# Kernel optimization log

Measured on AMD Instinct MI355X. Metric: run time of the kernel, lower is better.

The kernel has to match this reference:

```python
import jax, jax.numpy as jnp
import numpy as np

D_MODEL = 1024
N_HEADS = 16
D_K = D_MODEL // N_HEADS


def setup_inputs() -> dict:
    key = jax.random.key(0)
    kx, kq, kk, kv, ko = jax.random.split(key, 5)
    scale = 1.0 / np.sqrt(D_MODEL)
    return {
        "x": jax.random.normal(kx, (2, 2048, D_MODEL), dtype=jnp.float32),
        "W_Q": jax.random.normal(kq, (D_MODEL, D_MODEL), dtype=jnp.float32) * scale,
        "W_K": jax.random.normal(kk, (D_MODEL, D_MODEL), dtype=jnp.float32) * scale,
        "W_V": jax.random.normal(kv, (D_MODEL, D_MODEL), dtype=jnp.float32) * scale,
        "W_O": jax.random.normal(ko, (D_MODEL, D_MODEL), dtype=jnp.float32) * scale,
    }


def reference(x, W_Q, W_K, W_V, W_O) -> jnp.ndarray:
    B, S, _ = x.shape
    # Projections; weights stored as (d_model, d_model), applied as x @ W (Linear weight transposed convention folded into init)
    def heads(w):
        return jnp.einsum('bsd,de->bse', x, w).reshape(B, S, N_HEADS, D_K).transpose(0, 2, 1, 3)
    Q, K, V = heads(W_Q), heads(W_K), heads(W_V)  # (B,H,S,d_k)
    scores = jnp.einsum('bhqd,bhkd->bhqk', Q, K) / jnp.sqrt(jnp.asarray(D_K, x.dtype))
    causal_mask = jnp.triu(jnp.ones((S, S), dtype=bool), k=1)  # True above diagonal
    scores = jnp.where(causal_mask[None, None], jnp.asarray(-jnp.inf, x.dtype), scores)
    attn = jax.nn.softmax(scores, axis=-1)
    out = jnp.einsum('bhqk,bhkd->bhqd', attn, V)  # (B,H,S,d_k)
    out = out.transpose(0, 2, 1, 3).reshape(B, S, N_HEADS * D_K)
    return jnp.einsum('bsd,de->bse', out, W_O)
```

## Files before the change

### kernel.cpp

```cpp
#include <hip/hip_runtime.h>

typedef unsigned short u16;
typedef unsigned int u32;
typedef __attribute__((ext_vector_type(8))) __bf16 bf16x8;
typedef __attribute__((ext_vector_type(2))) __bf16 bf16x2;
typedef __attribute__((ext_vector_type(4))) float f32x4;
typedef __attribute__((ext_vector_type(16))) float f32x16;
typedef __attribute__((ext_vector_type(4))) u32 u32x4;

__device__ inline u16 f2bf(float f) {
  unsigned u = __builtin_bit_cast(unsigned, f);
  u += 0x7FFFu + ((u >> 16) & 1u);
  return (u16)(u >> 16);
}

__device__ inline u32 packbf(float a, float b) {
  bf16x2 t;
  t[0] = (__bf16)a;
  t[1] = (__bf16)b;
  return __builtin_bit_cast(u32, t);
}

__device__ inline void async16(const void* g, void* l) {
  __builtin_amdgcn_global_load_lds((const __attribute__((address_space(1))) void*)g,
                                   (__attribute__((address_space(3))) void*)l, 16, 0, 0);
}

__global__ __launch_bounds__(256) void xconv(const float* __restrict__ x, u16* __restrict__ xb) {
  int i = blockIdx.x * 256 + threadIdx.x;
  float4 v = ((const float4*)x)[i];
  ushort4 r;
  r.x = f2bf(v.x); r.y = f2bf(v.y); r.z = f2bf(v.z); r.w = f2bf(v.w);
  ((ushort4*)xb)[i] = r;
}

__global__ __launch_bounds__(256) void wtrans4(const float* __restrict__ W0,
                                               const float* __restrict__ W1,
                                               const float* __restrict__ W2,
                                               const float* __restrict__ W3,
                                               u16* __restrict__ WtQKV,
                                               u16* __restrict__ WtO) {
  __shared__ u16 tile[32][33];
  const int z = blockIdx.z;
  const float* W = (z == 0) ? W0 : (z == 1) ? W1 : (z == 2) ? W2 : W3;
  u16* Wt = (z < 3) ? (WtQKV + (size_t)z * 1024 * 1024) : WtO;
  const float s = (z == 0) ? 0.18033688011112042f : 1.0f;
  const int e0 = blockIdx.x * 32;
  const int d0 = blockIdx.y * 32;
  const int tx = threadIdx.x & 31;
  const int ty = threadIdx.x >> 5;
#pragma unroll
  for (int i = ty; i < 32; i += 8)
    tile[i][tx] = f2bf(W[(size_t)(d0 + i) * 1024 + e0 + tx] * s);
  __syncthreads();
#pragma unroll
  for (int i = ty; i < 32; i += 8)
    Wt[(size_t)(e0 + i) * 1024 + d0 + tx] = tile[tx][i];
}

__global__ __launch_bounds__(256) void vtrans(const u16* __restrict__ QKV, u16* __restrict__ Vtg) {
  __shared__ u16 t[32][66];
  const int tid = threadIdx.x;
  const int s0 = blockIdx.x * 32, dg0 = blockIdx.y * 64, b = blockIdx.z;
  {
    const int i = tid >> 3, c = (tid & 7) * 8;
    uint4 v = *(const uint4*)(QKV + (size_t)(b * 2048 + s0 + i) * 3072 + 2048 + dg0 + c);
    u16 tmp[8];
    *(uint4*)tmp = v;
#pragma unroll
    for (int e = 0; e < 8; ++e) t[i][c + e] = tmp[e];
  }
  __syncthreads();
  {
    const int r = tid >> 2, cg = (tid & 3) * 8;
    u16 tmp[8];
#pragma unroll
    for (int e = 0; e < 8; ++e) tmp[e] = t[cg + e][r];
    *(uint4*)(Vtg + (size_t)(b * 1024 + dg0 + r) * 2048 + s0 + cg) = *(uint4*)tmp;
  }
}

template <int OUT_BF16>
__global__ __launch_bounds__(256) void gemm_bt(const u16* __restrict__ A,
                                               const u16* __restrict__ Bt,
                                               void* __restrict__ Cp,
                                               int M, int N, int K) {
  __shared__ __align__(16) u16 As[128 * 32];
  __shared__ __align__(16) u16 Bs[128 * 32];
  const int tid = threadIdx.x;
  const int lane = tid & 63;
  const int wave = tid >> 6;
  const int lr = lane & 15;
  const int lk = (lane >> 4) * 8;
  const int wm = (wave >> 1) * 64;
  const int wn = (wave & 1) * 64;
  const int bm = blockIdx.x * 128;
  const int bn = blockIdx.y * 128;
  const int srow = lane >> 2;
  const int scol = (lane & 3) * 8;

  f32x4 acc[4][4] = {};

  for (int k0 = 0; k0 < K; k0 += 32) {
#pragma unroll
    for (int r = 0; r < 2; ++r) {
      const int chunk = r * 4 + wave;
      const int row = chunk * 16 + srow;
      async16(A + (size_t)(bm + row) * K + k0 + scol, &As[chunk * 512 + lane * 8]);
      async16(Bt + (size_t)(bn + row) * K + k0 + scol, &Bs[chunk * 512 + lane * 8]);
    }
    __syncthreads();
    bf16x8 a[4], b[4];
#pragma unroll
    for (int i = 0; i < 4; ++i) {
      a[i] = *(const bf16x8*)&As[(wm + i * 16 + lr) * 32 + lk];
      b[i] = *(const bf16x8*)&Bs[(wn + i * 16 + lr) * 32 + lk];
    }
#pragma unroll
    for (int mi = 0; mi < 4; ++mi)
#pragma unroll
      for (int ni = 0; ni < 4; ++ni)
        acc[mi][ni] = __builtin_amdgcn_mfma_f32_16x16x32_bf16(a[mi], b[ni], acc[mi][ni], 0, 0, 0);
    __syncthreads();
  }

#pragma unroll
  for (int mi = 0; mi < 4; ++mi) {
#pragma unroll
    for (int ni = 0; ni < 4; ++ni) {
      const int col = bn + wn + ni * 16 + lr;
#pragma unroll
      for (int j = 0; j < 4; ++j) {
        const int row = bm + wm + mi * 16 + (lane >> 4) * 4 + j;
        if (OUT_BF16)
          ((u16*)Cp)[(size_t)row * N + col] = f2bf(acc[mi][ni][j]);
        else
          ((float*)Cp)[(size_t)row * N + col] = acc[mi][ni][j];
      }
    }
  }
}

__global__ __launch_bounds__(512) void attn_kernel(const u16* __restrict__ QKV,
                                                   const u16* __restrict__ Vtg,
                                                   u16* __restrict__ Opart,
                                                   float* __restrict__ Lpart) {
  constexpr int S = 2048, LD = 3072;
  constexpr float MFIX = 12.0f;
  __shared__ __align__(16) u16 Ks[2][64 * 64];
  __shared__ __align__(16) u16 Vs[2][64 * 64];

  const int g = 7 - (blockIdx.x >> 1);
  const int c = blockIdx.x & 1;
  const int bh = blockIdx.y;
  const int b = bh >> 4, h = bh & 15;
  const int tid = threadIdx.x, lane = tid & 63, w = tid >> 6;
  const int l31 = lane & 31, lh = lane >> 5;

  const int qbase = g * 256 + w * 32;
  const int ktlast = 4 * g + (w >> 1);
  const int ktbeg = c * (2 * g + 2);
  const int ktend = (c + 1) * (2 * g + 2);

  const u16* qrow = QKV + (size_t)(b * S + qbase + l31) * LD + h * 64;
  bf16x8 qf[4];
#pragma unroll
  for (int cc = 0; cc < 4; ++cc) qf[cc] = *(const bf16x8*)(qrow + cc * 16 + lh * 8);

  const int r0 = tid >> 3, x0 = ((tid & 7) ^ (r0 & 7)) << 3;
  const u16* Kbase = QKV + (size_t)b * S * LD + 1024 + h * 64;
  const u16* Vbase = Vtg + (size_t)bh * 64 * 2048;

#define STAGE(buf, kt_)                                                          \
  do {                                                                           \
    async16(Kbase + (size_t)((kt_)*64 + r0) * LD + x0, &Ks[buf][tid * 8]);       \
    async16(Vbase + (size_t)r0 * 2048 + (kt_)*64 + x0, &Vs[buf][tid * 8]);       \
  } while (0)

  f32x16 o0 = {}, o1 = {};
  float l_run = 0.f;

  STAGE(0, ktbeg);

  int cur = 0;
  for (int kt = ktbeg; kt < ktend; ++kt) {
    if (kt + 1 < ktend) {
      STAGE(cur ^ 1, kt + 1);
      asm volatile("s_waitcnt vmcnt(2)" ::: "memory");
    } else {
      asm volatile("s_waitcnt vmcnt(0)" ::: "memory");
    }
    __builtin_amdgcn_s_barrier();
    __builtin_amdgcn_sched_barrier(0);

    const bool active = (kt <= ktlast);
    const bool hiA = active && ((kt < ktlast) || (w & 1));

    if (active) {
      const u16* ks = Ks[cur];
      const u16* vs = Vs[cur];

      f32x16 t0 = {}, t1 = {};
      __builtin_amdgcn_s_setprio(1);
#pragma unroll
      for (int cc = 0; cc < 4; ++cc) {
        const int ci = 2 * cc + lh;
        const bf16x8 kf0 = *(const bf16x8*)&ks[l31 * 64 + ((ci ^ (l31 & 7)) << 3)];
        t0 = __builtin_amdgcn_mfma_f32_32x32x16_bf16(kf0, qf[cc], t0, 0, 0, 0);
        if (hiA) {
          const bf16x8 kf1 = *(const bf16x8*)&ks[(32 + l31) * 64 + ((ci ^ (l31 & 7)) << 3)];
          t1 = __builtin_amdgcn_mfma_f32_32x32x16_bf16(kf1, qf[cc], t1, 0, 0, 0);
        }
      }
      __builtin_amdgcn_s_setprio(0);

      if (kt == ktlast) {
        const int kb = kt * 64 + 4 * lh;
        const int qa = qbase + l31;
#pragma unroll
        for (int r = 0; r < 16; ++r) {
          const int ko = (r & 3) + 8 * (r >> 2);
          if (kb + ko > qa) t0[r] = -3e38f;
          if (hiA && (kb + 32 + ko > qa)) t1[r] = -3e38f;
        }
      }

      f32x16 p0 = t0, p1 = t1;
#pragma unroll
      for (int r = 0; r < 16; ++r) p0[r] = exp2f(t0[r] - MFIX);
      if (hiA) {
#pragma unroll
        for (int r = 0; r < 16; ++r) p1[r] = exp2f(t1[r] - MFIX);
      }
      float v[16];
#pragma unroll
      for (int r = 0; r < 16; ++r) v[r] = hiA ? (p0[r] + p1[r]) : p0[r];
#pragma unroll
      for (int s = 8; s >= 1; s >>= 1)
#pragma unroll
        for (int r = 0; r < s; ++r) v[r] += v[r + s];
      l_run += v[0];

      u32 pk0[8], pk1[8], sw0[8], sw1[8];
#pragma unroll
      for (int j = 0; j < 8; ++j) pk0[j] = packbf(p0[2 * j], p0[2 * j + 1]);
#pragma unroll
      for (int j = 0; j < 8; ++j) sw0[j] = __shfl_xor(pk0[j], 32);
      if (hiA) {
#pragma unroll
        for (int j = 0; j < 8; ++j) pk1[j] = packbf(p1[2 * j], p1[2 * j + 1]);
#pragma unroll
        for (int j = 0; j < 8; ++j) sw1[j] = __shfl_xor(pk1[j], 32);
      }

      __builtin_amdgcn_s_setprio(1);
#define PVSTEP(kc, pk, sw)                                                             \
      {                                                                                \
        const int q4 = ((kc) & 1) * 4;                                                 \
        u32x4 wv;                                                                      \
        wv[0] = lh ? sw[q4 + 2] : pk[q4 + 0];                                          \
        wv[1] = lh ? sw[q4 + 3] : pk[q4 + 1];                                          \
        wv[2] = lh ? pk[q4 + 2] : sw[q4 + 0];                                          \
        wv[3] = lh ? pk[q4 + 3] : sw[q4 + 1];                                          \
        const bf16x8 pa = __builtin_bit_cast(bf16x8, wv);                              \
        const int ci = 2 * (kc) + lh;                                                  \
        const bf16x8 vf0 = *(const bf16x8*)&vs[l31 * 64 + ((ci ^ (l31 & 7)) << 3)];    \
        const bf16x8 vf1 = *(const bf16x8*)&vs[(32 + l31) * 64 + ((ci ^ (l31 & 7)) << 3)]; \
        o0 = __builtin_amdgcn_mfma_f32_32x32x16_bf16(pa, vf0, o0, 0, 0, 0);            \
        o1 = __builtin_amdgcn_mfma_f32_32x32x16_bf16(pa, vf1, o1, 0, 0, 0);            \
      }
      PVSTEP(0, pk0, sw0)
      PVSTEP(1, pk0, sw0)
      if (hiA) {
        PVSTEP(2, pk1, sw1)
        PVSTEP(3, pk1, sw1)
      }
#undef PVSTEP
      __builtin_amdgcn_s_setprio(0);
    }

    asm volatile("s_waitcnt lgkmcnt(0)" ::: "memory");
    __builtin_amdgcn_s_barrier();
    cur ^= 1;
  }
#undef STAGE

  u16* Oc = Opart + (size_t)c * 4096 * 1024;
#pragma unroll
  for (int r = 0; r < 16; ++r) {
    const int qo = (r & 3) + 8 * (r >> 2) + 4 * lh;
    u16* op = Oc + (size_t)(b * S + qbase + qo) * 1024 + h * 64 + l31;
    op[0] = f2bf(o0[r]);
    op[32] = f2bf(o1[r]);
  }
  const float l_tot = l_run + __shfl_xor(l_run, 32);
  if (lh == 0)
    Lpart[(size_t)c * 4096 * 16 + (size_t)(b * S + qbase + l31) * 16 + h] = l_tot;
}

__global__ __launch_bounds__(256) void combine(const u16* __restrict__ Opart,
                                               const float* __restrict__ Lpart,
                                               u16* __restrict__ Obuf) {
  const int i = blockIdx.x * 256 + threadIdx.x;
  const int row = i >> 7;
  const int cw = (i & 127) * 8;
  const int h = cw >> 6;
  const float l = Lpart[(size_t)row * 16 + h] + Lpart[(size_t)4096 * 16 + (size_t)row * 16 + h];
  const float inv = 1.0f / l;
  const bf16x8 a = *(const bf16x8*)(Opart + (size_t)row * 1024 + cw);
  const bf16x8 bq = *(const bf16x8*)(Opart + (size_t)4096 * 1024 + (size_t)row * 1024 + cw);
  u16 out[8];
#pragma unroll
  for (int j = 0; j < 8; ++j) out[j] = f2bf(((float)a[j] + (float)bq[j]) * inv);
  *(uint4*)(Obuf + (size_t)row * 1024 + cw) = *(uint4*)out;
}

extern "C" void kernel_launch(void* const* d_in, const int* in_sizes, int n_in,
                              void* d_out, int out_size, void* d_ws, size_t ws_size,
                              hipStream_t stream) {
  const float* x  = (const float*)d_in[0];
  const float* WQ = (const float*)d_in[1];
  const float* WK = (const float*)d_in[2];
  const float* WV = (const float*)d_in[3];
  const float* WO = (const float*)d_in[4];
  float* out = (float*)d_out;

  u16* xb    = (u16*)d_ws;
  u16* WtQKV = xb + (size_t)4096 * 1024;
  u16* WtO   = WtQKV + (size_t)3072 * 1024;
  u16* QKV   = WtO + (size_t)1024 * 1024;
  u16* Obuf  = QKV + (size_t)4096 * 3072;
  u16* Vtg   = Obuf + (size_t)4096 * 1024;
  u16* Opart = Vtg + (size_t)2048 * 2048;
  float* Lpart = (float*)(Opart + (size_t)2 * 4096 * 1024);

  xconv<<<4096, 256, 0, stream>>>(x, xb);
  wtrans4<<<dim3(32, 32, 4), 256, 0, stream>>>(WQ, WK, WV, WO, WtQKV, WtO);

  gemm_bt<1><<<dim3(32, 24), 256, 0, stream>>>(xb, WtQKV, QKV, 4096, 3072, 1024);
  vtrans<<<dim3(64, 16, 2), 256, 0, stream>>>(QKV, Vtg);
  attn_kernel<<<dim3(16, 32), 512, 0, stream>>>(QKV, Vtg, Opart, Lpart);
  combine<<<2048, 256, 0, stream>>>(Opart, Lpart, Obuf);
  gemm_bt<0><<<dim3(32, 8), 256, 0, stream>>>(Obuf, WtO, out, 4096, 1024, 1024);
}
```

Before: 164.9 us.

## Software-pipeline QK and softmax-PV across tiles and compute row sums via MFMA

The attention loop is restructured so the QK^T MFMAs for tile kt run alongside the softmax and PV of tile kt-1. V fragments are held in registers across iterations, and a drain step runs after the loop. Row sums are now produced by an extra MFMA against a ones vector instead of a scalar reduction. The per-warp causal skip logic is removed, so all tiles are computed and masked, which adds work on fully masked tiles. A launch-bounds occupancy hint of two blocks is also added, which raises register pressure.

```diff
diff --git a/kernel.cpp b/kernel.cpp
--- a/kernel.cpp
+++ b/kernel.cpp
@@ -141,10 +141,10 @@
   }
 }
 
-__global__ __launch_bounds__(512) void attn_kernel(const u16* __restrict__ QKV,
-                                                   const u16* __restrict__ Vtg,
-                                                   u16* __restrict__ Opart,
-                                                   float* __restrict__ Lpart) {
+__global__ __launch_bounds__(512, 2) void attn_kernel(const u16* __restrict__ QKV,
+                                                      const u16* __restrict__ Vtg,
+                                                      u16* __restrict__ Opart,
+                                                      float* __restrict__ Lpart) {
   constexpr int S = 2048, LD = 3072;
   constexpr float MFIX = 12.0f;
   __shared__ __align__(16) u16 Ks[2][64 * 64];
@@ -158,7 +158,7 @@
   const int l31 = lane & 31, lh = lane >> 5;
 
   const int qbase = g * 256 + w * 32;
-  const int ktlast = 4 * g + (w >> 1);
+  const int qa = qbase + l31;
   const int ktbeg = c * (2 * g + 2);
   const int ktend = (c + 1) * (2 * g + 2);
 
@@ -166,6 +166,13 @@
   bf16x8 qf[4];
 #pragma unroll
   for (int cc = 0; cc < 4; ++cc) qf[cc] = *(const bf16x8*)(qrow + cc * 16 + lh * 8);
+
+  bf16x8 onesf;
+  {
+    u32x4 ov;
+    ov[0] = ov[1] = ov[2] = ov[3] = 0x3F803F80u;
+    onesf = __builtin_bit_cast(bf16x8, ov);
+  }
 
   const int r0 = tid >> 3, x0 = ((tid & 7) ^ (r0 & 7)) << 3;
   const u16* Kbase = QKV + (size_t)b * S * LD + 1024 + h * 64;
@@ -178,9 +185,53 @@
   } while (0)
 
   f32x16 o0 = {}, o1 = {};
-  float l_run = 0.f;
+  f32x16 l_acc = {};
+  f32x16 tp0, tp1;
+#pragma unroll
+  for (int r = 0; r < 16; ++r) { tp0[r] = -3e38f; tp1[r] = -3e38f; }
+  bf16x8 vfp0[4], vfp1[4];
 
   STAGE(0, ktbeg);
+  asm volatile("s_waitcnt vmcnt(0)" ::: "memory");
+  __builtin_amdgcn_s_barrier();
+  __builtin_amdgcn_sched_barrier(0);
+#pragma unroll
+  for (int kc = 0; kc < 4; ++kc) {
+    const int ci = 2 * kc + lh;
+    vfp0[kc] = *(const bf16x8*)&Vs[0][l31 * 64 + ((ci ^ (l31 & 7)) << 3)];
+    vfp1[kc] = *(const bf16x8*)&Vs[0][(32 + l31) * 64 + ((ci ^ (l31 & 7)) << 3)];
+  }
+
+#define SOFTMAX_PV()                                                                   \
+  do {                                                                                 \
+    _Pragma("unroll") for (int r = 0; r < 16; ++r) {                                   \
+      tp0[r] = exp2f(tp0[r] - MFIX);                                                   \
+      tp1[r] = exp2f(tp1[r] - MFIX);                                                   \
+    }                                                                                  \
+    u32 pk0[8], pk1[8], sw0[8], sw1[8];                                                \
+    _Pragma("unroll") for (int j = 0; j < 8; ++j) {                                    \
+      pk0[j] = packbf(tp0[2 * j], tp0[2 * j + 1]);                                     \
+      pk1[j] = packbf(tp1[2 * j], tp1[2 * j + 1]);                                     \
+    }                                                                                  \
+    _Pragma("unroll") for (int j = 0; j < 8; ++j) {                                    \
+      sw0[j] = __shfl_xor(pk0[j], 32);                                                 \
+      sw1[j] = __shfl_xor(pk1[j], 32);                                                 \
+    }                                                                                  \
+    _Pragma("unroll") for (int kc = 0; kc < 4; ++kc) {                                 \
+      const u32* pk = (kc >> 1) ? pk1 : pk0;                                           \
+      const u32* sw = (kc >> 1) ? sw1 : sw0;                                           \
+      const int q4 = (kc & 1) * 4;                                                     \
+      u32x4 wv;                                                                        \
+      wv[0] = lh ? sw[q4 + 2] : pk[q4 + 0];                                            \
+      wv[1] = lh ? sw[q4 + 3] : pk[q4 + 1];                                            \
+      wv[2] = lh ? pk[q4 + 2] : sw[q4 + 0];                                            \
+      wv[3] = lh ? pk[q4 + 3] : sw[q4 + 1];                                            \
+      const bf16x8 pa = __builtin_bit_cast(bf16x8, wv);                                \
+      o0 = __builtin_amdgcn_mfma_f32_32x32x16_bf16(pa, vfp0[kc], o0, 0, 0, 0);         \
+      o1 = __builtin_amdgcn_mfma_f32_32x32x16_bf16(pa, vfp1[kc], o1, 0, 0, 0);         \
+      l_acc = __builtin_amdgcn_mfma_f32_32x32x16_bf16(pa, onesf, l_acc, 0, 0, 0);      \
+    }                                                                                  \
+  } while (0)
 
   int cur = 0;
   for (int kt = ktbeg; kt < ktend; ++kt) {
@@ -193,96 +244,46 @@
     __builtin_amdgcn_s_barrier();
     __builtin_amdgcn_sched_barrier(0);
 
-    const bool active = (kt <= ktlast);
-    const bool hiA = active && ((kt < ktlast) || (w & 1));
-
-    if (active) {
-      const u16* ks = Ks[cur];
-      const u16* vs = Vs[cur];
-
-      f32x16 t0 = {}, t1 = {};
-      __builtin_amdgcn_s_setprio(1);
-#pragma unroll
-      for (int cc = 0; cc < 4; ++cc) {
-        const int ci = 2 * cc + lh;
-        const bf16x8 kf0 = *(const bf16x8*)&ks[l31 * 64 + ((ci ^ (l31 & 7)) << 3)];
-        t0 = __builtin_amdgcn_mfma_f32_32x32x16_bf16(kf0, qf[cc], t0, 0, 0, 0);
-        if (hiA) {
-          const bf16x8 kf1 = *(const bf16x8*)&ks[(32 + l31) * 64 + ((ci ^ (l31 & 7)) << 3)];
-          t1 = __builtin_amdgcn_mfma_f32_32x32x16_bf16(kf1, qf[cc], t1, 0, 0, 0);
-        }
+    const u16* ks = Ks[cur];
+    const u16* vs = Vs[cur];
+
+    f32x16 tc0 = {}, tc1 = {};
+#pragma unroll
+    for (int cc = 0; cc < 4; ++cc) {
+      const int ci = 2 * cc + lh;
+      const bf16x8 kf0 = *(const bf16x8*)&ks[l31 * 64 + ((ci ^ (l31 & 7)) << 3)];
+      const bf16x8 kf1 = *(const bf16x8*)&ks[(32 + l31) * 64 + ((ci ^ (l31 & 7)) << 3)];
+      tc0 = __builtin_amdgcn_mfma_f32_32x32x16_bf16(kf0, qf[cc], tc0, 0, 0, 0);
+      tc1 = __builtin_amdgcn_mfma_f32_32x32x16_bf16(kf1, qf[cc], tc1, 0, 0, 0);
+    }
+    {
+      const int kb = kt * 64 + 4 * lh;
+#pragma unroll
+      for (int r = 0; r < 16; ++r) {
+        const int ko = kb + (r & 3) + 8 * (r >> 2);
+        tc0[r] = (ko > qa) ? -3e38f : tc0[r];
+        tc1[r] = (ko + 32 > qa) ? -3e38f : tc1[r];
       }
-      __builtin_amdgcn_s_setprio(0);
-
-      if (kt == ktlast) {
-        const int kb = kt * 64 + 4 * lh;
-        const int qa = qbase + l31;
-#pragma unroll
-        for (int r = 0; r < 16; ++r) {
-          const int ko = (r & 3) + 8 * (r >> 2);
-          if (kb + ko > qa) t0[r] = -3e38f;
-          if (hiA && (kb + 32 + ko > qa)) t1[r] = -3e38f;
-        }
-      }
-
-      f32x16 p0 = t0, p1 = t1;
-#pragma unroll
-      for (int r = 0; r < 16; ++r) p0[r] = exp2f(t0[r] - MFIX);
-      if (hiA) {
-#pragma unroll
-        for (int r = 0; r < 16; ++r) p1[r] = exp2f(t1[r] - MFIX);
-      }
-      float v[16];
-#pragma unroll
-      for (int r = 0; r < 16; ++r) v[r] = hiA ? (p0[r] + p1[r]) : p0[r];
-#pragma unroll
-      for (int s = 8; s >= 1; s >>= 1)
-#pragma unroll
-        for (int r = 0; r < s; ++r) v[r] += v[r + s];
-      l_run += v[0];
-
-      u32 pk0[8], pk1[8], sw0[8], sw1[8];
-#pragma unroll
-      for (int j = 0; j < 8; ++j) pk0[j] = packbf(p0[2 * j], p0[2 * j + 1]);
-#pragma unroll
-      for (int j = 0; j < 8; ++j) sw0[j] = __shfl_xor(pk0[j], 32);
-      if (hiA) {
-#pragma unroll
-        for (int j = 0; j < 8; ++j) pk1[j] = packbf(p1[2 * j], p1[2 * j + 1]);
-#pragma unroll
-        for (int j = 0; j < 8; ++j) sw1[j] = __shfl_xor(pk1[j], 32);
-      }
-
-      __builtin_amdgcn_s_setprio(1);
-#define PVSTEP(kc, pk, sw)                                                             \
-      {                                                                                \
-        const int q4 = ((kc) & 1) * 4;                                                 \
-        u32x4 wv;                                                                      \
-        wv[0] = lh ? sw[q4 + 2] : pk[q4 + 0];                                          \
-        wv[1] = lh ? sw[q4 + 3] : pk[q4 + 1];                                          \
-        wv[2] = lh ? pk[q4 + 2] : sw[q4 + 0];                                          \
-        wv[3] = lh ? pk[q4 + 3] : sw[q4 + 1];                                          \
-        const bf16x8 pa = __builtin_bit_cast(bf16x8, wv);                              \
-        const int ci = 2 * (kc) + lh;                                                  \
-        const bf16x8 vf0 = *(const bf16x8*)&vs[l31 * 64 + ((ci ^ (l31 & 7)) << 3)];    \
-        const bf16x8 vf1 = *(const bf16x8*)&vs[(32 + l31) * 64 + ((ci ^ (l31 & 7)) << 3)]; \
-        o0 = __builtin_amdgcn_mfma_f32_32x32x16_bf16(pa, vf0, o0, 0, 0, 0);            \
-        o1 = __builtin_amdgcn_mfma_f32_32x32x16_bf16(pa, vf1, o1, 0, 0, 0);            \
-      }
-      PVSTEP(0, pk0, sw0)
-      PVSTEP(1, pk0, sw0)
-      if (hiA) {
-        PVSTEP(2, pk1, sw1)
-        PVSTEP(3, pk1, sw1)
-      }
-#undef PVSTEP
-      __builtin_amdgcn_s_setprio(0);
-    }
+    }
+
+    SOFTMAX_PV();
+
+#pragma unroll
+    for (int kc = 0; kc < 4; ++kc) {
+      const int ci = 2 * kc + lh;
+      vfp0[kc] = *(const bf16x8*)&vs[l31 * 64 + ((ci ^ (l31 & 7)) << 3)];
+      vfp1[kc] = *(const bf16x8*)&vs[(32 + l31) * 64 + ((ci ^ (l31 & 7)) << 3)];
+    }
+    tp0 = tc0;
+    tp1 = tc1;
 
     asm volatile("s_waitcnt lgkmcnt(0)" ::: "memory");
     __builtin_amdgcn_s_barrier();
     cur ^= 1;
   }
+
+  SOFTMAX_PV();
+#undef SOFTMAX_PV
 #undef STAGE
 
   u16* Oc = Opart + (size_t)c * 4096 * 1024;
@@ -293,9 +294,13 @@
     op[0] = f2bf(o0[r]);
     op[32] = f2bf(o1[r]);
   }
-  const float l_tot = l_run + __shfl_xor(l_run, 32);
-  if (lh == 0)
-    Lpart[(size_t)c * 4096 * 16 + (size_t)(b * S + qbase + l31) * 16 + h] = l_tot;
+  if (l31 == 0) {
+#pragma unroll
+    for (int r = 0; r < 16; ++r) {
+      const int qo = (r & 3) + 8 * (r >> 2) + 4 * lh;
+      Lpart[(size_t)c * 4096 * 16 + (size_t)(b * S + qbase + qo) * 16 + h] = l_acc[r];
+    }
+  }
 }
 
 __global__ __launch_bounds__(256) void combine(const u16* __restrict__ Opart,
```

New measurement: 170.0 us. 1.03x slower.

## Give each attention wave 64 query rows to reuse K/V fragments

Applied to the files above, without the earlier changes.

Halves the attention block to 256 threads (4 waves), with each wave now owning 64 query rows as two 32-row halves instead of 32 rows. Each K and V fragment read from LDS then feeds twice as many MFMAs. Each thread issues twice as many async copies per stage, and the causal mask on the diagonal tile is simplified to a local comparison. In exchange, per-wave register pressure roughly doubles (four output accumulators, two Q fragment sets) and each block has fewer waves, which may reduce occupancy and latency hiding.

```diff
diff --git a/kernel.cpp b/kernel.cpp
--- a/kernel.cpp
+++ b/kernel.cpp
@@ -141,10 +141,10 @@
   }
 }
 
-__global__ __launch_bounds__(512) void attn_kernel(const u16* __restrict__ QKV,
-                                                   const u16* __restrict__ Vtg,
-                                                   u16* __restrict__ Opart,
-                                                   float* __restrict__ Lpart) {
+__global__ __launch_bounds__(256, 2) void attn_kernel(const u16* __restrict__ QKV,
+                                                      const u16* __restrict__ Vtg,
+                                                      u16* __restrict__ Opart,
+                                                      float* __restrict__ Lpart) {
   constexpr int S = 2048, LD = 3072;
   constexpr float MFIX = 12.0f;
   __shared__ __align__(16) u16 Ks[2][64 * 64];
@@ -157,28 +157,55 @@
   const int tid = threadIdx.x, lane = tid & 63, w = tid >> 6;
   const int l31 = lane & 31, lh = lane >> 5;
 
-  const int qbase = g * 256 + w * 32;
-  const int ktlast = 4 * g + (w >> 1);
+  const int qbase = g * 256 + w * 64;
+  const int ktlast = 4 * g + w;
   const int ktbeg = c * (2 * g + 2);
   const int ktend = (c + 1) * (2 * g + 2);
 
-  const u16* qrow = QKV + (size_t)(b * S + qbase + l31) * LD + h * 64;
-  bf16x8 qf[4];
-#pragma unroll
-  for (int cc = 0; cc < 4; ++cc) qf[cc] = *(const bf16x8*)(qrow + cc * 16 + lh * 8);
-
-  const int r0 = tid >> 3, x0 = ((tid & 7) ^ (r0 & 7)) << 3;
+  bf16x8 qf[2][4];
+#pragma unroll
+  for (int qh = 0; qh < 2; ++qh) {
+    const u16* qrow = QKV + (size_t)(b * S + qbase + qh * 32 + l31) * LD + h * 64;
+#pragma unroll
+    for (int cc = 0; cc < 4; ++cc) qf[qh][cc] = *(const bf16x8*)(qrow + cc * 16 + lh * 8);
+  }
+
+  const int c0 = tid, c1 = tid + 256;
+  const int r0 = c0 >> 3, x0 = ((c0 & 7) ^ (r0 & 7)) << 3;
+  const int r1 = c1 >> 3, x1 = ((c1 & 7) ^ (r1 & 7)) << 3;
   const u16* Kbase = QKV + (size_t)b * S * LD + 1024 + h * 64;
   const u16* Vbase = Vtg + (size_t)bh * 64 * 2048;
 
 #define STAGE(buf, kt_)                                                          \
   do {                                                                           \
-    async16(Kbase + (size_t)((kt_)*64 + r0) * LD + x0, &Ks[buf][tid * 8]);       \
-    async16(Vbase + (size_t)r0 * 2048 + (kt_)*64 + x0, &Vs[buf][tid * 8]);       \
+    async16(Kbase + (size_t)((kt_)*64 + r0) * LD + x0, &Ks[buf][c0 * 8]);        \
+    async16(Kbase + (size_t)((kt_)*64 + r1) * LD + x1, &Ks[buf][c1 * 8]);        \
+    async16(Vbase + (size_t)r0 * 2048 + (kt_)*64 + x0, &Vs[buf][c0 * 8]);        \
+    async16(Vbase + (size_t)r1 * 2048 + (kt_)*64 + x1, &Vs[buf][c1 * 8]);        \
   } while (0)
 
-  f32x16 o0 = {}, o1 = {};
-  float l_run = 0.f;
+  f32x16 o00 = {}, o01 = {}, o10 = {}, o11 = {};
+  float l0 = 0.f, l1 = 0.f;
+
+#define TREE16(dst, arr)                                                         \
+  do {                                                                           \
+    float v_[16];                                                                \
+    _Pragma("unroll") for (int r_ = 0; r_ < 16; ++r_) v_[r_] = (arr)[r_];        \
+    _Pragma("unroll") for (int s_ = 8; s_ >= 1; s_ >>= 1)                        \
+      _Pragma("unroll") for (int r_ = 0; r_ < s_; ++r_) v_[r_] += v_[r_ + s_];   \
+    dst += v_[0];                                                                \
+  } while (0)
+
+#define MAKE_PA(pa, pk, sw, q4)                                                  \
+  bf16x8 pa;                                                                     \
+  {                                                                              \
+    u32x4 wv_;                                                                   \
+    wv_[0] = lh ? (sw)[(q4) + 2] : (pk)[(q4) + 0];                               \
+    wv_[1] = lh ? (sw)[(q4) + 3] : (pk)[(q4) + 1];                               \
+    wv_[2] = lh ? (pk)[(q4) + 2] : (sw)[(q4) + 0];                               \
+    wv_[3] = lh ? (pk)[(q4) + 3] : (sw)[(q4) + 1];                               \
+    pa = __builtin_bit_cast(bf16x8, wv_);                                        \
+  }
 
   STAGE(0, ktbeg);
 
@@ -186,7 +213,7 @@
   for (int kt = ktbeg; kt < ktend; ++kt) {
     if (kt + 1 < ktend) {
       STAGE(cur ^ 1, kt + 1);
-      asm volatile("s_waitcnt vmcnt(2)" ::: "memory");
+      asm volatile("s_waitcnt vmcnt(4)" ::: "memory");
     } else {
       asm volatile("s_waitcnt vmcnt(0)" ::: "memory");
     }
@@ -194,88 +221,100 @@
     __builtin_amdgcn_sched_barrier(0);
 
     const bool active = (kt <= ktlast);
-    const bool hiA = active && ((kt < ktlast) || (w & 1));
-
     if (active) {
+      const bool full = (kt < ktlast);
       const u16* ks = Ks[cur];
       const u16* vs = Vs[cur];
 
-      f32x16 t0 = {}, t1 = {};
+      f32x16 t00 = {}, t10 = {}, t01 = {}, t11 = {};
       __builtin_amdgcn_s_setprio(1);
 #pragma unroll
       for (int cc = 0; cc < 4; ++cc) {
         const int ci = 2 * cc + lh;
         const bf16x8 kf0 = *(const bf16x8*)&ks[l31 * 64 + ((ci ^ (l31 & 7)) << 3)];
-        t0 = __builtin_amdgcn_mfma_f32_32x32x16_bf16(kf0, qf[cc], t0, 0, 0, 0);
-        if (hiA) {
-          const bf16x8 kf1 = *(const bf16x8*)&ks[(32 + l31) * 64 + ((ci ^ (l31 & 7)) << 3)];
-          t1 = __builtin_amdgcn_mfma_f32_32x32x16_bf16(kf1, qf[cc], t1, 0, 0, 0);
+        const bf16x8 kf1 = *(const bf16x8*)&ks[(32 + l31) * 64 + ((ci ^ (l31 & 7)) << 3)];
+        t00 = __builtin_amdgcn_mfma_f32_32x32x16_bf16(kf0, qf[0][cc], t00, 0, 0, 0);
+        t01 = __builtin_amdgcn_mfma_f32_32x32x16_bf16(kf0, qf[1][cc], t01, 0, 0, 0);
+        if (full) t10 = __builtin_amdgcn_mfma_f32_32x32x16_bf16(kf1, qf[0][cc], t10, 0, 0, 0);
+        t11 = __builtin_amdgcn_mfma_f32_32x32x16_bf16(kf1, qf[1][cc], t11, 0, 0, 0);
+      }
+      __builtin_amdgcn_s_setprio(0);
+
+      if (!full) {
+#pragma unroll
+        for (int r = 0; r < 16; ++r) {
+          const int ko = (r & 3) + 8 * (r >> 2) + 4 * lh;
+          if (ko > l31) { t00[r] = -3e38f; t11[r] = -3e38f; }
         }
       }
+
+      u32 pk0[8], pk1[8], sw0[8], sw1[8];
+
+#pragma unroll
+      for (int r = 0; r < 16; ++r) t00[r] = exp2f(t00[r] - MFIX);
+#pragma unroll
+      for (int r = 0; r < 16; ++r) t01[r] = exp2f(t01[r] - MFIX);
+      TREE16(l0, t00);
+      TREE16(l1, t01);
+#pragma unroll
+      for (int j = 0; j < 8; ++j) {
+        pk0[j] = packbf(t00[2 * j], t00[2 * j + 1]);
+        pk1[j] = packbf(t01[2 * j], t01[2 * j + 1]);
+      }
+#pragma unroll
+      for (int j = 0; j < 8; ++j) {
+        sw0[j] = __shfl_xor(pk0[j], 32);
+        sw1[j] = __shfl_xor(pk1[j], 32);
+      }
+      __builtin_amdgcn_s_setprio(1);
+#pragma unroll
+      for (int kc = 0; kc < 2; ++kc) {
+        const int q4 = kc * 4;
+        MAKE_PA(pa0, pk0, sw0, q4)
+        MAKE_PA(pa1, pk1, sw1, q4)
+        const int ci = 2 * kc + lh;
+        const bf16x8 vd0 = *(const bf16x8*)&vs[l31 * 64 + ((ci ^ (l31 & 7)) << 3)];
+        const bf16x8 vd1 = *(const bf16x8*)&vs[(32 + l31) * 64 + ((ci ^ (l31 & 7)) << 3)];
+        o00 = __builtin_amdgcn_mfma_f32_32x32x16_bf16(pa0, vd0, o00, 0, 0, 0);
+        o01 = __builtin_amdgcn_mfma_f32_32x32x16_bf16(pa0, vd1, o01, 0, 0, 0);
+        o10 = __builtin_amdgcn_mfma_f32_32x32x16_bf16(pa1, vd0, o10, 0, 0, 0);
+        o11 = __builtin_amdgcn_mfma_f32_32x32x16_bf16(pa1, vd1, o11, 0, 0, 0);
+      }
       __builtin_amdgcn_s_setprio(0);
 
-      if (kt == ktlast) {
-        const int kb = kt * 64 + 4 * lh;
-        const int qa = qbase + l31;
-#pragma unroll
-        for (int r = 0; r < 16; ++r) {
-          const int ko = (r & 3) + 8 * (r >> 2);
-          if (kb + ko > qa) t0[r] = -3e38f;
-          if (hiA && (kb + 32 + ko > qa)) t1[r] = -3e38f;
+      if (full) {
+#pragma unroll
+        for (int r = 0; r < 16; ++r) t10[r] = exp2f(t10[r] - MFIX);
+        TREE16(l0, t10);
+#pragma unroll
+        for (int j = 0; j < 8; ++j) pk0[j] = packbf(t10[2 * j], t10[2 * j + 1]);
+#pragma unroll
+        for (int j = 0; j < 8; ++j) sw0[j] = __shfl_xor(pk0[j], 32);
+      }
+#pragma unroll
+      for (int r = 0; r < 16; ++r) t11[r] = exp2f(t11[r] - MFIX);
+      TREE16(l1, t11);
+#pragma unroll
+      for (int j = 0; j < 8; ++j) pk1[j] = packbf(t11[2 * j], t11[2 * j + 1]);
+#pragma unroll
+      for (int j = 0; j < 8; ++j) sw1[j] = __shfl_xor(pk1[j], 32);
+
+      __builtin_amdgcn_s_setprio(1);
+#pragma unroll
+      for (int kc = 0; kc < 2; ++kc) {
+        const int q4 = kc * 4;
+        MAKE_PA(pa1, pk1, sw1, q4)
+        const int ci = 2 * (kc + 2) + lh;
+        const bf16x8 vd0 = *(const bf16x8*)&vs[l31 * 64 + ((ci ^ (l31 & 7)) << 3)];
+        const bf16x8 vd1 = *(const bf16x8*)&vs[(32 + l31) * 64 + ((ci ^ (l31 & 7)) << 3)];
+        if (full) {
+          MAKE_PA(pa0, pk0, sw0, q4)
+          o00 = __builtin_amdgcn_mfma_f32_32x32x16_bf16(pa0, vd0, o00, 0, 0, 0);
+          o01 = __builtin_amdgcn_mfma_f32_32x32x16_bf16(pa0, vd1, o01, 0, 0, 0);
         }
-      }
-
-      f32x16 p0 = t0, p1 = t1;
-#pragma unroll
-      for (int r = 0; r < 16; ++r) p0[r] = exp2f(t0[r] - MFIX);
-      if (hiA) {
-#pragma unroll
-        for (int r = 0; r < 16; ++r) p1[r] = exp2f(t1[r] - MFIX);
-      }
-      float v[16];
-#pragma unroll
-      for (int r = 0; r < 16; ++r) v[r] = hiA ? (p0[r] + p1[r]) : p0[r];
-#pragma unroll
-      for (int s = 8; s >= 1; s >>= 1)
-#pragma unroll
-        for (int r = 0; r < s; ++r) v[r] += v[r + s];
-      l_run += v[0];
-
-      u32 pk0[8], pk1[8], sw0[8], sw1[8];
-#pragma unroll
-      for (int j = 0; j < 8; ++j) pk0[j] = packbf(p0[2 * j], p0[2 * j + 1]);
-#pragma unroll
-      for (int j = 0; j < 8; ++j) sw0[j] = __shfl_xor(pk0[j], 32);
-      if (hiA) {
-#pragma unroll
-        for (int j = 0; j < 8; ++j) pk1[j] = packbf(p1[2 * j], p1[2 * j + 1]);
-#pragma unroll
-        for (int j = 0; j < 8; ++j) sw1[j] = __shfl_xor(pk1[j], 32);
-      }
-
-      __builtin_amdgcn_s_setprio(1);
-#define PVSTEP(kc, pk, sw)                                                             \
-      {                                                                                \
-        const int q4 = ((kc) & 1) * 4;                                                 \
-        u32x4 wv;                                                                      \
-        wv[0] = lh ? sw[q4 + 2] : pk[q4 + 0];                                          \
-        wv[1] = lh ? sw[q4 + 3] : pk[q4 + 1];                                          \
-        wv[2] = lh ? pk[q4 + 2] : sw[q4 + 0];                                          \
-        wv[3] = lh ? pk[q4 + 3] : sw[q4 + 1];                                          \
-        const bf16x8 pa = __builtin_bit_cast(bf16x8, wv);                              \
-        const int ci = 2 * (kc) + lh;                                                  \
-        const bf16x8 vf0 = *(const bf16x8*)&vs[l31 * 64 + ((ci ^ (l31 & 7)) << 3)];    \
-        const bf16x8 vf1 = *(const bf16x8*)&vs[(32 + l31) * 64 + ((ci ^ (l31 & 7)) << 3)]; \
-        o0 = __builtin_amdgcn_mfma_f32_32x32x16_bf16(pa, vf0, o0, 0, 0, 0);            \
-        o1 = __builtin_amdgcn_mfma_f32_32x32x16_bf16(pa, vf1, o1, 0, 0, 0);            \
-      }
-      PVSTEP(0, pk0, sw0)
-      PVSTEP(1, pk0, sw0)
-      if (hiA) {
-        PVSTEP(2, pk1, sw1)
-        PVSTEP(3, pk1, sw1)
-      }
-#undef PVSTEP
+        o10 = __builtin_amdgcn_mfma_f32_32x32x16_bf16(pa1, vd0, o10, 0, 0, 0);
+        o11 = __builtin_amdgcn_mfma_f32_32x32x16_bf16(pa1, vd1, o11, 0, 0, 0);
+      }
       __builtin_amdgcn_s_setprio(0);
     }
 
@@ -284,18 +323,26 @@
     cur ^= 1;
   }
 #undef STAGE
-
+#undef TREE16
+#undef MAKE_PA
+
+  const float l0t = l0 + __shfl_xor(l0, 32);
+  const float l1t = l1 + __shfl_xor(l1, 32);
   u16* Oc = Opart + (size_t)c * 4096 * 1024;
 #pragma unroll
   for (int r = 0; r < 16; ++r) {
     const int qo = (r & 3) + 8 * (r >> 2) + 4 * lh;
-    u16* op = Oc + (size_t)(b * S + qbase + qo) * 1024 + h * 64 + l31;
-    op[0] = f2bf(o0[r]);
-    op[32] = f2bf(o1[r]);
-  }
-  const float l_tot = l_run + __shfl_xor(l_run, 32);
-  if (lh == 0)
-    Lpart[(size_t)c * 4096 * 16 + (size_t)(b * S + qbase + l31) * 16 + h] = l_tot;
+    u16* p0 = Oc + (size_t)(b * S + qbase + qo) * 1024 + h * 64 + l31;
+    u16* p1 = p0 + (size_t)32 * 1024;
+    p0[0] = f2bf(o00[r]);
+    p0[32] = f2bf(o01[r]);
+    p1[0] = f2bf(o10[r]);
+    p1[32] = f2bf(o11[r]);
+  }
+  if (lh == 0) {
+    Lpart[(size_t)c * 4096 * 16 + (size_t)(b * S + qbase + l31) * 16 + h] = l0t;
+    Lpart[(size_t)c * 4096 * 16 + (size_t)(b * S + qbase + 32 + l31) * 16 + h] = l1t;
+  }
 }
 
 __global__ __launch_bounds__(256) void combine(const u16* __restrict__ Opart,
@@ -339,7 +386,7 @@
 
   gemm_bt<1><<<dim3(32, 24), 256, 0, stream>>>(xb, WtQKV, QKV, 4096, 3072, 1024);
   vtrans<<<dim3(64, 16, 2), 256, 0, stream>>>(QKV, Vtg);
-  attn_kernel<<<dim3(16, 32), 512, 0, stream>>>(QKV, Vtg, Opart, Lpart);
+  attn_kernel<<<dim3(16, 32), 256, 0, stream>>>(QKV, Vtg, Opart, Lpart);
   combine<<<2048, 256, 0, stream>>>(Opart, Lpart, Obuf);
   gemm_bt<0><<<dim3(32, 8), 256, 0, stream>>>(Obuf, WtO, out, 4096, 1024, 1024);
 }
```

Measured after the change: 147.5 us. 1.12x faster.
